# Kernel optimization log

Hardware: AMD Instinct MI355X
Metric: run time of the kernel (lower is better)

## Reference

```python
import jax, jax.numpy as jnp
import numpy as np

N_STEP = 6
MODULUS = 1.0
BN_EPS = 1e-5
B, LS, M, LW, LY, HID = 64, 256, 4, 256, 128, 512
D_IN = 2 * LS + 2 * LW + LY  # 1152


def setup_inputs() -> dict:
    key = jax.random.key(0)
    ks = jax.random.split(key, 12)
    phi = jax.random.normal(ks[0], (B, LS), jnp.float32)
    w_real = jax.random.normal(ks[1], (B, LW, M), jnp.float32)
    w_imag = jax.random.normal(ks[2], (B, LW, M), jnp.float32)
    y = jax.random.normal(ks[3], (B, LY, M), jnp.float32)
    G_real = jax.random.normal(ks[4], (B, LS, LS, M), jnp.float32)
    G_imag = jax.random.normal(ks[5], (B, LS, LS, M), jnp.float32)
    # H must give well-conditioned s^H H s: build Hermitian PD H = A A^H / Ls + I
    Ar = jax.random.normal(ks[6], (B, LS, LS, M), jnp.float32)
    Ai = jax.random.normal(ks[7], (B, LS, LS, M), jnp.float32)
    A = (Ar + 1j * Ai).astype(jnp.complex64)
    H = jnp.einsum('bikm,bjkm->bijm', A, jnp.conj(A)) / LS
    H = H + jnp.eye(LS, dtype=jnp.complex64)[None, :, :, None]
    H_real = jnp.real(H).astype(jnp.float32)
    H_imag = jnp.imag(H).astype(jnp.float32)
    W1 = jax.random.normal(ks[8], (D_IN, HID), jnp.float32) * (1.0 / np.sqrt(D_IN))
    b1 = jnp.zeros((HID,), jnp.float32)
    gamma = jnp.ones((HID,), jnp.float32)
    beta = jnp.zeros((HID,), jnp.float32)
    W2 = jax.random.normal(ks[9], (HID,), jnp.float32) * (1.0 / np.sqrt(HID))
    b2 = jnp.zeros((), jnp.float32)
    return {"phi": phi, "w_real": w_real, "w_imag": w_imag, "y": y,
            "G_real": G_real, "G_imag": G_imag, "H_real": H_real, "H_imag": H_imag,
            "W1": W1, "b1": b1, "gamma": gamma, "beta": beta, "W2": W2, "b2": b2}


def reference(phi, w_real, w_imag, y, G_real, G_imag, H_real, H_imag,
              W1, b1, gamma, beta, W2, b2):
    G = (G_real + 1j * G_imag).astype(jnp.complex64)  # [B,Ls,Ls,M]
    H = (H_real + 1j * H_imag).astype(jnp.complex64)
    # per-target static features of the rho-MLP input: [B, M, 2*Lw+Ly]
    wy = jnp.concatenate([jnp.transpose(w_real, (0, 2, 1)),
                          jnp.transpose(w_imag, (0, 2, 1)),
                          jnp.transpose(y, (0, 2, 1))], axis=-1)

    s_list, rho_list = [], []
    for _ in range(N_STEP):
        s = MODULUS * jnp.exp(1j * phi).astype(jnp.complex64)  # [B,Ls]
        sc = jnp.conj(s)
        # quadratic-form matvecs, vectorized over targets m
        Gs = jnp.einsum('bijm,bj->bim', G, s)                 # [B,Ls,M]
        Hs = jnp.einsum('bijm,bj->bim', H, s)
        sGs = jnp.einsum('bi,bim->bm', sc, Gs)                # [B,M]
        sHs = jnp.einsum('bi,bim->bm', sc, Hs)
        # eta_sred_bn, per target: [B,Ls,M]
        num = (sHs[:, None, :] * Gs - sGs[:, None, :] * Hs) * sc[:, :, None]
        eta = jnp.real(2.0 / sHs[:, None, :] ** 2 * jnp.imag(num))
        # rho MLP with BatchNorm (batch stats over axis 0), per target
        s_feat = jnp.broadcast_to(
            jnp.concatenate([jnp.real(s), jnp.imag(s)], axis=-1)[:, None, :],
            (s.shape[0], M, 2 * LS))
        X = jnp.concatenate([s_feat, wy], axis=-1)            # [B,M,D_in]
        h = jnp.einsum('bmd,dh->bmh', X, W1) + b1
        mu = jnp.mean(h, axis=0, keepdims=True)
        var = jnp.var(h, axis=0, keepdims=True)
        h = gamma * (h - mu) * jax.lax.rsqrt(var + BN_EPS) + beta
        h = jax.nn.relu(h)
        rho = jax.nn.sigmoid(jnp.einsum('bmh,h->bm', h, W2) + b2)  # [B,M]
        eta_net = jnp.sum(eta * rho[:, None, :], axis=-1)          # [B,Ls]
        phi = phi - eta_net
        s_list.append(s)
        rho_list.append(rho)
    s_list.append(MODULUS * jnp.exp(1j * phi).astype(jnp.complex64))
    s_stack = jnp.stack(s_list, axis=1)        # [B,N_step+1,Ls] complex64
    rho_stack = jnp.stack(rho_list, axis=1)    # [B,N_step,M]
    return jnp.real(s_stack), jnp.imag(s_stack), rho_stack
```

## Files before the change

### kernel.cpp

```cpp
#include <hip/hip_runtime.h>
#include <math.h>

typedef float f4 __attribute__((ext_vector_type(4)));

constexpr int kB = 64;
constexpr int kLs = 256;
constexpr int kM = 4;
constexpr int kLw = 256;
constexpr int kLy = 128;
constexpr int kHid = 512;
constexpr int kSteps = 6;
constexpr float kEps = 1e-5f;

__device__ __forceinline__ float wred(float v) {
#pragma unroll
  for (int off = 32; off > 0; off >>= 1) v += __shfl_down(v, off, 64);
  return v;
}

__global__ __launch_bounds__(256) void k_static(
    const float* __restrict__ wr, const float* __restrict__ wi,
    const float* __restrict__ yy, const float* __restrict__ W1,
    const float* __restrict__ b1, float* __restrict__ hstat) {
  const int b = blockIdx.x >> 1;
  const int hid = ((blockIdx.x & 1) << 8) + threadIdx.x;
  const float* w1c = W1 + hid;
  f4 acc = {0.f, 0.f, 0.f, 0.f};
#pragma unroll 4
  for (int l = 0; l < kLw; ++l) {
    const float w1v = w1c[(size_t)(2 * kLs + l) * kHid];
    const f4 w = *(const f4*)(wr + ((size_t)b * kLw + l) * kM);
#pragma unroll
    for (int m = 0; m < kM; ++m) acc[m] += w[m] * w1v;
  }
#pragma unroll 4
  for (int l = 0; l < kLw; ++l) {
    const float w1v = w1c[(size_t)(2 * kLs + kLw + l) * kHid];
    const f4 w = *(const f4*)(wi + ((size_t)b * kLw + l) * kM);
#pragma unroll
    for (int m = 0; m < kM; ++m) acc[m] += w[m] * w1v;
  }
#pragma unroll 4
  for (int l = 0; l < kLy; ++l) {
    const float w1v = w1c[(size_t)(2 * kLs + 2 * kLw + l) * kHid];
    const f4 w = *(const f4*)(yy + ((size_t)b * kLy + l) * kM);
#pragma unroll
    for (int m = 0; m < kM; ++m) acc[m] += w[m] * w1v;
  }
  const float bv = b1[hid];
#pragma unroll
  for (int m = 0; m < kM; ++m)
    hstat[((size_t)b * kM + m) * kHid + hid] = acc[m] + bv;
}

__global__ __launch_bounds__(256) void k_s0(
    const float* __restrict__ phi, float* __restrict__ sReg,
    float* __restrict__ sImg, float* __restrict__ outSR,
    float* __restrict__ outSI) {
  const int b = blockIdx.x, t = threadIdx.x;
  float sn, cs;
  sincosf(phi[b * kLs + t], &sn, &cs);
  sReg[b * kLs + t] = cs;
  sImg[b * kLs + t] = sn;
  const size_t oo = ((size_t)b * (kSteps + 1)) * kLs + t;
  outSR[oo] = cs;
  outSI[oo] = sn;
}

typedef struct {
  f4 gr[4], gi[4], hr[4], hi[4];
} RowBuf;

__device__ __forceinline__ void load_row(RowBuf& rb, const float* __restrict__ grp,
                                         const float* __restrict__ gip,
                                         const float* __restrict__ hrp,
                                         const float* __restrict__ hip_, int r) {
#pragma unroll
  for (int rr = 0; rr < 4; ++rr) {
    const size_t off = (size_t)r * (kLs * kM) + (size_t)(rr * 64) * kM;
    rb.gr[rr] = *(const f4*)(grp + off);
    rb.gi[rr] = *(const f4*)(gip + off);
    rb.hr[rr] = *(const f4*)(hrp + off);
    rb.hi[rr] = *(const f4*)(hip_ + off);
  }
}

__device__ __forceinline__ void compute_row(
    const RowBuf& rb, const float* s_r, const float* s_i,
    float* __restrict__ gsR, float* __restrict__ gsI,
    float* __restrict__ hsR, float* __restrict__ hsI,
    size_t obase, int r, int lane) {
  f4 aGr = {0, 0, 0, 0}, aGi = {0, 0, 0, 0};
  f4 aHr = {0, 0, 0, 0}, aHi = {0, 0, 0, 0};
#pragma unroll
  for (int rr = 0; rr < 4; ++rr) {
    const float sr = s_r[rr], si = s_i[rr];
#pragma unroll
    for (int m = 0; m < kM; ++m) {
      aGr[m] += rb.gr[rr][m] * sr - rb.gi[rr][m] * si;
      aGi[m] += rb.gr[rr][m] * si + rb.gi[rr][m] * sr;
      aHr[m] += rb.hr[rr][m] * sr - rb.hi[rr][m] * si;
      aHi[m] += rb.hr[rr][m] * si + rb.hi[rr][m] * sr;
    }
  }
#pragma unroll
  for (int m = 0; m < kM; ++m) {
    aGr[m] = wred(aGr[m]);
    aGi[m] = wred(aGi[m]);
    aHr[m] = wred(aHr[m]);
    aHi[m] = wred(aHi[m]);
  }
  if (lane == 0) {
    const size_t o = obase + (size_t)r * kM;
    *(f4*)(gsR + o) = aGr;
    *(f4*)(gsI + o) = aGi;
    *(f4*)(hsR + o) = aHr;
    *(f4*)(hsI + o) = aHi;
  }
}

__global__ __launch_bounds__(256, 2) void k_step_main(
    const float* __restrict__ Gr, const float* __restrict__ Gi,
    const float* __restrict__ Hr, const float* __restrict__ Hi,
    const float* __restrict__ W1, const float* __restrict__ sReg,
    const float* __restrict__ sImg, float* __restrict__ gsR,
    float* __restrict__ gsI, float* __restrict__ hsR,
    float* __restrict__ hsI, float* __restrict__ hdyn) {
  const int t = threadIdx.x;
  const int blk = blockIdx.x;

  if (blk < kB * 2) {
    const int b = blk >> 1;
    const int hid = ((blk & 1) << 8) + t;
    const float* w1c = W1 + hid;
    const float* sr = sReg + b * kLs;
    const float* si = sImg + b * kLs;
    float acc = 0.f;
#pragma unroll 8
    for (int j = 0; j < kLs; ++j) {
      acc += sr[j] * w1c[(size_t)j * kHid];
      acc += si[j] * w1c[(size_t)(j + kLs) * kHid];
    }
    hdyn[b * kHid + hid] = acc;
    return;
  }

  const int mb = blk - kB * 2;
  const int lane = t & 63;
  const int wv = t >> 6;
  const int b = mb >> 3;
  const int i0 = ((mb & 7) << 5) + (wv << 3);
  const size_t row0 = ((size_t)b * kLs + i0) * (kLs * kM) + (size_t)lane * kM;
  const float* grp = Gr + row0;
  const float* gip = Gi + row0;
  const float* hrp = Hr + row0;
  const float* hip_ = Hi + row0;
  const size_t obase = ((size_t)b * kLs + i0) * kM;

  RowBuf A, B;
  load_row(A, grp, gip, hrp, hip_, 0);
  float s_r[4], s_i[4];
#pragma unroll
  for (int rr = 0; rr < 4; ++rr) {
    s_r[rr] = sReg[b * kLs + (rr << 6) + lane];
    s_i[rr] = sImg[b * kLs + (rr << 6) + lane];
  }
  __builtin_amdgcn_sched_barrier(0);
#pragma unroll
  for (int r = 0; r < 8; r += 2) {
    load_row(B, grp, gip, hrp, hip_, r + 1);
    __builtin_amdgcn_sched_barrier(0);
    compute_row(A, s_r, s_i, gsR, gsI, hsR, hsI, obase, r, lane);
    __builtin_amdgcn_sched_barrier(0);
    if (r + 2 < 8) {
      load_row(A, grp, gip, hrp, hip_, r + 2);
      __builtin_amdgcn_sched_barrier(0);
    }
    compute_row(B, s_r, s_i, gsR, gsI, hsR, hsI, obase, r + 1, lane);
    __builtin_amdgcn_sched_barrier(0);
  }
}

__global__ __launch_bounds__(256) void k_bn(
    const float* __restrict__ hdyn, const float* __restrict__ hstat,
    float* __restrict__ mu_g, float* __restrict__ rs_g) {
  const int q = blockIdx.x * 256 + threadIdx.x;
  const int m = q >> 9;
  const int hid = q & (kHid - 1);
  float sum = 0.f, ss = 0.f;
#pragma unroll 8
  for (int bb = 0; bb < kB; ++bb) {
    const float h = hdyn[bb * kHid + hid] + hstat[((size_t)bb * kM + m) * kHid + hid];
    sum += h;
    ss += h * h;
  }
  const float mu = sum * (1.f / kB);
  const float var = ss * (1.f / kB) - mu * mu;
  mu_g[q] = mu;
  rs_g[q] = rsqrtf(var + kEps);
}

__global__ __launch_bounds__(256) void k_step_finish(
    const float* __restrict__ gsR, const float* __restrict__ gsI,
    const float* __restrict__ hsR, const float* __restrict__ hsI,
    const float* __restrict__ hdyn, const float* __restrict__ hstat,
    const float* __restrict__ mu_g, const float* __restrict__ rs_g,
    const float* __restrict__ gamma_, const float* __restrict__ beta_,
    const float* __restrict__ W2, const float* __restrict__ b2,
    float* __restrict__ phi, float* __restrict__ sReg, float* __restrict__ sImg,
    float* __restrict__ outSR, float* __restrict__ outSI,
    float* __restrict__ outRho, int step) {
  const int b = blockIdx.x, t = threadIdx.x;
  const int lane = t & 63, wv = t >> 6;
  __shared__ float red[4][16];
  __shared__ float sgR[4], sgI[4], shR[4], shI[4], c2[4];
  __shared__ float rho_s[4];

  const int idx = b * kLs + t;
  const float p = phi[idx];
  const float cs = sReg[idx];
  const float sn = sImg[idx];

  const size_t o = (size_t)idx * kM;
  const f4 gR = *(const f4*)(gsR + o);
  const f4 gI = *(const f4*)(gsI + o);
  const f4 hR = *(const f4*)(hsR + o);
  const f4 hI = *(const f4*)(hsI + o);

  float v[16];
#pragma unroll
  for (int m = 0; m < kM; ++m) {
    v[m] = cs * gR[m] + sn * gI[m];
    v[4 + m] = cs * gI[m] - sn * gR[m];
    v[8 + m] = cs * hR[m] + sn * hI[m];
    v[12 + m] = cs * hI[m] - sn * hR[m];
  }
#pragma unroll
  for (int k = 0; k < 16; ++k) v[k] = wred(v[k]);
  if (lane == 0) {
#pragma unroll
    for (int k = 0; k < 16; ++k) red[wv][k] = v[k];
  }
  __syncthreads();
  if (t == 0) {
#pragma unroll
    for (int m = 0; m < kM; ++m) {
      const float gr = red[0][m] + red[1][m] + red[2][m] + red[3][m];
      const float gi = red[0][4 + m] + red[1][4 + m] + red[2][4 + m] + red[3][4 + m];
      const float hr = red[0][8 + m] + red[1][8 + m] + red[2][8 + m] + red[3][8 + m];
      const float hi = red[0][12 + m] + red[1][12 + m] + red[2][12 + m] + red[3][12 + m];
      sgR[m] = gr; sgI[m] = gi; shR[m] = hr; shI[m] = hi;
      const float xr = hr * hr - hi * hi;
      const float xi = 2.f * hr * hi;
      c2[m] = 2.f * xr / (xr * xr + xi * xi);
    }
  }
  __syncthreads();

  float pm[4] = {0.f, 0.f, 0.f, 0.f};
#pragma unroll
  for (int kk = 0; kk < 2; ++kk) {
    const int hid = (kk << 8) + t;
    const float hd = hdyn[b * kHid + hid];
    const float ga = gamma_[hid], be = beta_[hid], w2 = W2[hid];
#pragma unroll
    for (int m = 0; m < kM; ++m) {
      const float h = hd + hstat[((size_t)b * kM + m) * kHid + hid];
      const int q = m * kHid + hid;
      float hn = ga * (h - mu_g[q]) * rs_g[q] + be;
      hn = fmaxf(hn, 0.f);
      pm[m] += hn * w2;
    }
  }
#pragma unroll
  for (int m = 0; m < kM; ++m) pm[m] = wred(pm[m]);
  if (lane == 0) {
#pragma unroll
    for (int m = 0; m < kM; ++m) red[wv][m] = pm[m];
  }
  __syncthreads();
  if (t < 4) {
    const float tot = red[0][t] + red[1][t] + red[2][t] + red[3][t] + b2[0];
    const float r = 1.f / (1.f + expf(-tot));
    rho_s[t] = r;
    outRho[((size_t)b * kSteps + step) * kM + t] = r;
  }
  __syncthreads();

  float en = 0.f;
#pragma unroll
  for (int m = 0; m < kM; ++m) {
    const float ar = shR[m] * gR[m] - shI[m] * gI[m] - (sgR[m] * hR[m] - sgI[m] * hI[m]);
    const float ai = shR[m] * gI[m] + shI[m] * gR[m] - (sgR[m] * hI[m] + sgI[m] * hR[m]);
    en += c2[m] * (ai * cs - ar * sn) * rho_s[m];
  }
  const float pn = p - en;
  phi[idx] = pn;
  float sn2, cs2;
  sincosf(pn, &sn2, &cs2);
  sReg[idx] = cs2;
  sImg[idx] = sn2;
  const size_t oo = ((size_t)b * (kSteps + 1) + step + 1) * kLs + t;
  outSR[oo] = cs2;
  outSI[oo] = sn2;
}

extern "C" void kernel_launch(void* const* d_in, const int* in_sizes, int n_in,
                              void* d_out, int out_size, void* d_ws, size_t ws_size,
                              hipStream_t stream) {
  const float* phi_in = (const float*)d_in[0];
  const float* w_real = (const float*)d_in[1];
  const float* w_imag = (const float*)d_in[2];
  const float* y = (const float*)d_in[3];
  const float* G_real = (const float*)d_in[4];
  const float* G_imag = (const float*)d_in[5];
  const float* H_real = (const float*)d_in[6];
  const float* H_imag = (const float*)d_in[7];
  const float* W1 = (const float*)d_in[8];
  const float* b1 = (const float*)d_in[9];
  const float* gamma_ = (const float*)d_in[10];
  const float* beta_ = (const float*)d_in[11];
  const float* W2 = (const float*)d_in[12];
  const float* b2 = (const float*)d_in[13];

  float* ws = (float*)d_ws;
  float* phi = ws;
  float* gsR = phi + kB * kLs;
  float* gsI = gsR + kB * kLs * kM;
  float* hsR = gsI + kB * kLs * kM;
  float* hsI = hsR + kB * kLs * kM;
  float* hdyn = hsI + kB * kLs * kM;
  float* hstat = hdyn + kB * kHid;
  float* mu_g = hstat + (size_t)kB * kM * kHid;
  float* rs_g = mu_g + kM * kHid;
  float* sReg = rs_g + kM * kHid;
  float* sImg = sReg + kB * kLs;

  float* out = (float*)d_out;
  float* outSR = out;
  float* outSI = out + (size_t)kB * (kSteps + 1) * kLs;
  float* outRho = out + 2 * (size_t)kB * (kSteps + 1) * kLs;

  hipMemcpyAsync(phi, phi_in, (size_t)kB * kLs * sizeof(float),
                 hipMemcpyDeviceToDevice, stream);
  k_static<<<dim3(kB * 2), dim3(256), 0, stream>>>(w_real, w_imag, y, W1, b1, hstat);
  k_s0<<<dim3(kB), dim3(256), 0, stream>>>(phi, sReg, sImg, outSR, outSI);
  for (int step = 0; step < kSteps; ++step) {
    k_step_main<<<dim3(kB * 2 + kB * kLs / 32), dim3(256), 0, stream>>>(
        G_real, G_imag, H_real, H_imag, W1, sReg, sImg, gsR, gsI, hsR, hsI, hdyn);
    k_bn<<<dim3(kM * kHid / 256), dim3(256), 0, stream>>>(hdyn, hstat, mu_g, rs_g);
    k_step_finish<<<dim3(kB), dim3(256), 0, stream>>>(
        gsR, gsI, hsR, hsI, hdyn, hstat, mu_g, rs_g, gamma_, beta_, W2, b2,
        phi, sReg, sImg, outSR, outSI, outRho, step);
  }
}
```

Measured before the change: 646.8 us.

## Split G/H matvec into two rows per wave across more blocks

The G·s and H·s matvec work is redistributed. Each wave now handles 2 rows instead of 8, and the grid grows from 512 to 2048 matvec blocks. Each row is processed as separate G and H passes with a short two-register software pipeline, replacing the double-buffered 64-register RowBuf scheme, and the launch-bounds occupancy hint is dropped. The intent is more waves in flight and lower register pressure to hide memory latency on this bandwidth-bound stream. The cost is more blocks, more reductions per byte, and less per-wave prefetch depth.

```diff
diff --git a/kernel.cpp b/kernel.cpp
--- a/kernel.cpp
+++ b/kernel.cpp
@@ -67,59 +67,7 @@
   outSI[oo] = sn;
 }
 
-typedef struct {
-  f4 gr[4], gi[4], hr[4], hi[4];
-} RowBuf;
-
-__device__ __forceinline__ void load_row(RowBuf& rb, const float* __restrict__ grp,
-                                         const float* __restrict__ gip,
-                                         const float* __restrict__ hrp,
-                                         const float* __restrict__ hip_, int r) {
-#pragma unroll
-  for (int rr = 0; rr < 4; ++rr) {
-    const size_t off = (size_t)r * (kLs * kM) + (size_t)(rr * 64) * kM;
-    rb.gr[rr] = *(const f4*)(grp + off);
-    rb.gi[rr] = *(const f4*)(gip + off);
-    rb.hr[rr] = *(const f4*)(hrp + off);
-    rb.hi[rr] = *(const f4*)(hip_ + off);
-  }
-}
-
-__device__ __forceinline__ void compute_row(
-    const RowBuf& rb, const float* s_r, const float* s_i,
-    float* __restrict__ gsR, float* __restrict__ gsI,
-    float* __restrict__ hsR, float* __restrict__ hsI,
-    size_t obase, int r, int lane) {
-  f4 aGr = {0, 0, 0, 0}, aGi = {0, 0, 0, 0};
-  f4 aHr = {0, 0, 0, 0}, aHi = {0, 0, 0, 0};
-#pragma unroll
-  for (int rr = 0; rr < 4; ++rr) {
-    const float sr = s_r[rr], si = s_i[rr];
-#pragma unroll
-    for (int m = 0; m < kM; ++m) {
-      aGr[m] += rb.gr[rr][m] * sr - rb.gi[rr][m] * si;
-      aGi[m] += rb.gr[rr][m] * si + rb.gi[rr][m] * sr;
-      aHr[m] += rb.hr[rr][m] * sr - rb.hi[rr][m] * si;
-      aHi[m] += rb.hr[rr][m] * si + rb.hi[rr][m] * sr;
-    }
-  }
-#pragma unroll
-  for (int m = 0; m < kM; ++m) {
-    aGr[m] = wred(aGr[m]);
-    aGi[m] = wred(aGi[m]);
-    aHr[m] = wred(aHr[m]);
-    aHi[m] = wred(aHi[m]);
-  }
-  if (lane == 0) {
-    const size_t o = obase + (size_t)r * kM;
-    *(f4*)(gsR + o) = aGr;
-    *(f4*)(gsI + o) = aGi;
-    *(f4*)(hsR + o) = aHr;
-    *(f4*)(hsI + o) = aHi;
-  }
-}
-
-__global__ __launch_bounds__(256, 2) void k_step_main(
+__global__ __launch_bounds__(256) void k_step_main(
     const float* __restrict__ Gr, const float* __restrict__ Gi,
     const float* __restrict__ Hr, const float* __restrict__ Hi,
     const float* __restrict__ W1, const float* __restrict__ sReg,
@@ -148,37 +96,67 @@
   const int mb = blk - kB * 2;
   const int lane = t & 63;
   const int wv = t >> 6;
-  const int b = mb >> 3;
-  const int i0 = ((mb & 7) << 5) + (wv << 3);
-  const size_t row0 = ((size_t)b * kLs + i0) * (kLs * kM) + (size_t)lane * kM;
-  const float* grp = Gr + row0;
-  const float* gip = Gi + row0;
-  const float* hrp = Hr + row0;
-  const float* hip_ = Hi + row0;
-  const size_t obase = ((size_t)b * kLs + i0) * kM;
-
-  RowBuf A, B;
-  load_row(A, grp, gip, hrp, hip_, 0);
+  const int gw = (mb << 2) + wv;
+  const int row0 = gw << 1;
+  const int b = row0 >> 8;
+
   float s_r[4], s_i[4];
 #pragma unroll
   for (int rr = 0; rr < 4; ++rr) {
-    s_r[rr] = sReg[b * kLs + (rr << 6) + lane];
-    s_i[rr] = sImg[b * kLs + (rr << 6) + lane];
-  }
-  __builtin_amdgcn_sched_barrier(0);
-#pragma unroll
-  for (int r = 0; r < 8; r += 2) {
-    load_row(B, grp, gip, hrp, hip_, r + 1);
-    __builtin_amdgcn_sched_barrier(0);
-    compute_row(A, s_r, s_i, gsR, gsI, hsR, hsI, obase, r, lane);
-    __builtin_amdgcn_sched_barrier(0);
-    if (r + 2 < 8) {
-      load_row(A, grp, gip, hrp, hip_, r + 2);
-      __builtin_amdgcn_sched_barrier(0);
-    }
-    compute_row(B, s_r, s_i, gsR, gsI, hsR, hsI, obase, r + 1, lane);
-    __builtin_amdgcn_sched_barrier(0);
-  }
+    s_r[rr] = sReg[(b << 8) + (rr << 6) + lane];
+    s_i[rr] = sImg[(b << 8) + (rr << 6) + lane];
+  }
+
+  auto pass = [&](const float* __restrict__ pr, const float* __restrict__ pi,
+                  float* __restrict__ oR, float* __restrict__ oI,
+                  size_t rb) {
+    f4 cr0, ci0, cr1, ci1;
+    cr0 = *(const f4*)(pr + rb);
+    ci0 = *(const f4*)(pi + rb);
+    f4 aR = {0, 0, 0, 0}, aI = {0, 0, 0, 0};
+    cr1 = *(const f4*)(pr + rb + 256);
+    ci1 = *(const f4*)(pi + rb + 256);
+#pragma unroll
+    for (int m = 0; m < kM; ++m) {
+      aR[m] += cr0[m] * s_r[0] - ci0[m] * s_i[0];
+      aI[m] += cr0[m] * s_i[0] + ci0[m] * s_r[0];
+    }
+    cr0 = *(const f4*)(pr + rb + 512);
+    ci0 = *(const f4*)(pi + rb + 512);
+#pragma unroll
+    for (int m = 0; m < kM; ++m) {
+      aR[m] += cr1[m] * s_r[1] - ci1[m] * s_i[1];
+      aI[m] += cr1[m] * s_i[1] + ci1[m] * s_r[1];
+    }
+    cr1 = *(const f4*)(pr + rb + 768);
+    ci1 = *(const f4*)(pi + rb + 768);
+#pragma unroll
+    for (int m = 0; m < kM; ++m) {
+      aR[m] += cr0[m] * s_r[2] - ci0[m] * s_i[2];
+      aI[m] += cr0[m] * s_i[2] + ci0[m] * s_r[2];
+    }
+#pragma unroll
+    for (int m = 0; m < kM; ++m) {
+      aR[m] += cr1[m] * s_r[3] - ci1[m] * s_i[3];
+      aI[m] += cr1[m] * s_i[3] + ci1[m] * s_r[3];
+    }
+#pragma unroll
+    for (int m = 0; m < kM; ++m) {
+      aR[m] = wred(aR[m]);
+      aI[m] = wred(aI[m]);
+    }
+    if (lane == 0) {
+      *(f4*)oR = aR;
+      *(f4*)oI = aI;
+    }
+  };
+
+  const size_t base = (size_t)row0 * (kLs * kM) + (size_t)(lane << 2);
+  const size_t o0 = (size_t)row0 * kM;
+  pass(Gr, Gi, gsR + o0, gsI + o0, base);
+  pass(Hr, Hi, hsR + o0, hsI + o0, base);
+  pass(Gr, Gi, gsR + o0 + kM, gsI + o0 + kM, base + kLs * kM);
+  pass(Hr, Hi, hsR + o0 + kM, hsI + o0 + kM, base + kLs * kM);
 }
 
 __global__ __launch_bounds__(256) void k_bn(
@@ -346,7 +324,7 @@
   k_static<<<dim3(kB * 2), dim3(256), 0, stream>>>(w_real, w_imag, y, W1, b1, hstat);
   k_s0<<<dim3(kB), dim3(256), 0, stream>>>(phi, sReg, sImg, outSR, outSI);
   for (int step = 0; step < kSteps; ++step) {
-    k_step_main<<<dim3(kB * 2 + kB * kLs / 32), dim3(256), 0, stream>>>(
+    k_step_main<<<dim3(kB * 2 + 2048), dim3(256), 0, stream>>>(
         G_real, G_imag, H_real, H_imag, W1, sReg, sImg, gsR, gsI, hsR, hsI, hdyn);
     k_bn<<<dim3(kM * kHid / 256), dim3(256), 0, stream>>>(hdyn, hstat, mu_g, rs_g);
     k_step_finish<<<dim3(kB), dim3(256), 0, stream>>>(
```

Result: faster. 623.1 us (-3.7%).
